# Performance work log

Hardware: AMD Instinct MI355X
Metric: run time of the kernel (lower is better)

The kernel has to match this reference:

```python
import math
import jax, jax.numpy as jnp
import numpy as np

SHAPES = ((100, 150), (50, 75), (25, 38), (13, 19))  # (H, W) per level
N_HEADS = 8
N_POINTS = 4
EMBED = 256


def setup_inputs() -> dict:
    key = jax.random.key(0)
    ks = jax.random.split(key, 8)
    bs = 2
    L = len(SHAPES)
    nv = sum(h * w for h, w in SHAPES)  # 19947
    nq = nv
    d = EMBED
    query = jax.random.normal(ks[0], (bs, nq, d), jnp.float32)
    value = jax.random.normal(ks[1], (bs, nv, d), jnp.float32)
    reference_points = jax.random.uniform(ks[2], (bs, nq, L, 2), dtype=jnp.float32)
    spatial_shapes = jnp.asarray(np.array(SHAPES, np.int32))
    # sampling_offsets bias: directional grid init, as in the module's init_weights
    thetas = np.arange(N_HEADS, dtype=np.float64) * (2.0 * math.pi / N_HEADS)
    grid = np.stack([np.cos(thetas), np.sin(thetas)], -1)
    grid = grid / np.abs(grid).max(-1, keepdims=True)
    grid = np.tile(grid[:, None, None, :], (1, L, N_POINTS, 1))
    grid = grid * np.arange(1, N_POINTS + 1, dtype=np.float64)[None, None, :, None]
    b_off = jnp.asarray(grid.reshape(-1), jnp.float32)  # (h*L*p*2,)
    # small random weights (zero-init in module would make offsets constant)
    W_off = 0.01 * jax.random.normal(ks[3], (N_HEADS * L * N_POINTS * 2, d), jnp.float32)
    W_attn = 0.01 * jax.random.normal(ks[4], (N_HEADS * L * N_POINTS, d), jnp.float32)
    b_attn = jnp.zeros((N_HEADS * L * N_POINTS,), jnp.float32)
    s = 1.0 / math.sqrt(d)
    W_val = s * jax.random.normal(ks[5], (d, d), jnp.float32)
    b_val = jnp.zeros((d,), jnp.float32)
    W_out = s * jax.random.normal(ks[6], (d, d), jnp.float32)
    b_out = jnp.zeros((d,), jnp.float32)
    return dict(query=query, value=value, reference_points=reference_points,
                spatial_shapes=spatial_shapes, W_off=W_off, b_off=b_off,
                W_attn=W_attn, b_attn=b_attn, W_val=W_val, b_val=b_val,
                W_out=W_out, b_out=b_out)


def _msda(value, shapes, loc, attn):
    """Multi-scale deformable attention core.
    value: (bs, nv, h, hd)  loc: (bs, nq, h, L, p, 2) in [0,1]
    attn:  (bs, nq, h, L, p) -> returns (bs, nq, h*hd)
    Equivalent to grid_sample(bilinear, padding='zeros', align_corners=False).
    """
    bs, nq, h, L, p, _ = loc.shape
    hd = value.shape[-1]
    out = jnp.zeros((bs, nq, h, hd), value.dtype)
    start = 0
    for lvl in range(L):
        H, W = int(shapes[lvl, 0]), int(shapes[lvl, 1])
        v = value[:, start:start + H * W]               # (bs, H*W, h, hd)
        l = loc[:, :, :, lvl]                           # (bs, nq, h, p, 2)
        # align_corners=False unnormalization: x = loc*W - 0.5
        x = l[..., 0] * W - 0.5
        y = l[..., 1] * H - 0.5
        x0 = jnp.floor(x)
        y0 = jnp.floor(y)
        wx = x - x0
        wy = y - y0
        x0i = x0.astype(jnp.int32)
        y0i = y0.astype(jnp.int32)

        def corner(xi, yi, w):
            valid = (xi >= 0) & (xi < W) & (yi >= 0) & (yi < H)
            idx = jnp.clip(yi, 0, H - 1) * W + jnp.clip(xi, 0, W - 1)  # (bs,nq,h,p)
            idxf = idx.transpose(0, 1, 3, 2).reshape(bs, nq * p, h)
            g = jnp.take_along_axis(v, idxf[..., None], axis=1)        # (bs,nq*p,h,hd)
            g = g.reshape(bs, nq, p, h, hd).transpose(0, 1, 3, 2, 4)   # (bs,nq,h,p,hd)
            return g * jnp.where(valid, w, 0.0)[..., None]

        samp = (corner(x0i, y0i, (1 - wx) * (1 - wy))
                + corner(x0i + 1, y0i, wx * (1 - wy))
                + corner(x0i, y0i + 1, (1 - wx) * wy)
                + corner(x0i + 1, y0i + 1, wx * wy))
        out = out + (samp * attn[:, :, :, lvl, :, None]).sum(3)
        start += H * W
    return out.reshape(bs, nq, h * hd)


def reference(query, value, reference_points, spatial_shapes,
              W_off, b_off, W_attn, b_attn, W_val, b_val, W_out, b_out):
    shapes = np.asarray(spatial_shapes)  # static level shapes
    bs, nq, d = query.shape
    L = shapes.shape[0]
    h, p = N_HEADS, N_POINTS
    hd = d // h
    off = (query @ W_off.T + b_off).reshape(bs, nq, h, L, p, 2)
    aw = (query @ W_attn.T + b_attn).reshape(bs, nq, h, L * p)
    aw = jax.nn.softmax(aw, axis=-1).reshape(bs, nq, h, L, p)
    v = (value @ W_val.T + b_val).reshape(bs, -1, h, hd)
    # offset normalizer is (W, H) per level
    norm = jnp.asarray(np.stack([shapes[:, 1], shapes[:, 0]], -1), query.dtype)  # (L,2)
    loc = reference_points[:, :, None, :, None, :] + off / norm[None, None, None, :, None, :]
    out = _msda(v, shapes, loc, aw)          # (bs, nq, d)
    return out @ W_out.T + b_out
```

## Files before the change

kernel.cpp:

```cpp
#include <hip/hip_runtime.h>
#include <hip/hip_bf16.h>
#include <hip/hip_fp16.h>
#include <cmath>


typedef __attribute__((ext_vector_type(8))) short short8;
typedef __attribute__((ext_vector_type(4))) float f32x4;

#define MREAL 39894
#define MP    39936
#define NQ2   39894

__device__ __forceinline__ unsigned short f2bf(float f) {
    union { float f; unsigned u; } x; x.f = f;
    unsigned r = (x.u + 0x7fffu + ((x.u >> 16) & 1u)) >> 16;
    return (unsigned short)r;
}
__device__ __forceinline__ unsigned cvt_pk_bf16(float lo, float hi) {
    unsigned r;
    asm("v_cvt_pk_bf16_f32 %0, %1, %2" : "=v"(r) : "v"(lo), "v"(hi));
    return r;
}

template<int AMODE, int OUTMODE>
__device__ __forceinline__ void gemm_body(
    short* As, short* Bs,
    const void* A, const float* B1, const float* B2, int nsplit,
    const float* bias, const float* bias2, int bsplit,
    void* Cout, int ldc, int m_t, int n_t, int Mstore)
{
    const int tid = threadIdx.x;
    const int m0 = m_t * 128;
    const int n0 = n_t * 128;
    const int w  = tid >> 6;
    const int l  = tid & 63;
    const int wm = w >> 1, wn = w & 1;

    const int sr  = tid >> 2;
    const int skc = (tid & 3) * 8;

    const int lr = l & 15;
    const int lk = (l >> 4) * 8;

    const int br0 = n0 + sr, br1 = n0 + sr + 64;
    const float* Bp0 = (br0 < nsplit) ? B1 + (size_t)br0 * 256
                                      : B2 + (size_t)(br0 - nsplit) * 256;
    const float* Bp1 = (br1 < nsplit) ? B1 + (size_t)br1 * 256
                                      : B2 + (size_t)(br1 - nsplit) * 256;

    f32x4 acc[4][4] = {};

    for (int k0 = 0; k0 < 256; k0 += 32) {
        __syncthreads();
        if constexpr (AMODE == 0) {
            const short* Ab = (const short*)A;
            *reinterpret_cast<short8*>(&As[sr * 40 + skc]) =
                *reinterpret_cast<const short8*>(&Ab[(size_t)(m0 + sr) * 256 + k0 + skc]);
            *reinterpret_cast<short8*>(&As[(sr + 64) * 40 + skc]) =
                *reinterpret_cast<const short8*>(&Ab[(size_t)(m0 + sr + 64) * 256 + k0 + skc]);
        } else {
            const float* Af = (const float*)A;
            const int r0 = min(m0 + sr, MREAL - 1);
            const int r1 = min(m0 + sr + 64, MREAL - 1);
            float4 a0 = *reinterpret_cast<const float4*>(&Af[(size_t)r0 * 256 + k0 + skc]);
            float4 a1 = *reinterpret_cast<const float4*>(&Af[(size_t)r0 * 256 + k0 + skc + 4]);
            float4 b0 = *reinterpret_cast<const float4*>(&Af[(size_t)r1 * 256 + k0 + skc]);
            float4 b1 = *reinterpret_cast<const float4*>(&Af[(size_t)r1 * 256 + k0 + skc + 4]);
            uint4 pa, pb;
            pa.x = cvt_pk_bf16(a0.x, a0.y); pa.y = cvt_pk_bf16(a0.z, a0.w);
            pa.z = cvt_pk_bf16(a1.x, a1.y); pa.w = cvt_pk_bf16(a1.z, a1.w);
            pb.x = cvt_pk_bf16(b0.x, b0.y); pb.y = cvt_pk_bf16(b0.z, b0.w);
            pb.z = cvt_pk_bf16(b1.x, b1.y); pb.w = cvt_pk_bf16(b1.z, b1.w);
            *reinterpret_cast<uint4*>(&As[sr * 40 + skc]) = pa;
            *reinterpret_cast<uint4*>(&As[(sr + 64) * 40 + skc]) = pb;
        }
        {
            float4 c0 = *reinterpret_cast<const float4*>(Bp0 + k0 + skc);
            float4 c1 = *reinterpret_cast<const float4*>(Bp0 + k0 + skc + 4);
            float4 d0 = *reinterpret_cast<const float4*>(Bp1 + k0 + skc);
            float4 d1 = *reinterpret_cast<const float4*>(Bp1 + k0 + skc + 4);
            uint4 pc, pd;
            pc.x = cvt_pk_bf16(c0.x, c0.y); pc.y = cvt_pk_bf16(c0.z, c0.w);
            pc.z = cvt_pk_bf16(c1.x, c1.y); pc.w = cvt_pk_bf16(c1.z, c1.w);
            pd.x = cvt_pk_bf16(d0.x, d0.y); pd.y = cvt_pk_bf16(d0.z, d0.w);
            pd.z = cvt_pk_bf16(d1.x, d1.y); pd.w = cvt_pk_bf16(d1.z, d1.w);
            *reinterpret_cast<uint4*>(&Bs[sr * 40 + skc]) = pc;
            *reinterpret_cast<uint4*>(&Bs[(sr + 64) * 40 + skc]) = pd;
        }
        __syncthreads();

        short8 bfr[4];
#pragma unroll
        for (int ni = 0; ni < 4; ++ni)
            bfr[ni] = *reinterpret_cast<const short8*>(&Bs[(wn * 64 + ni * 16 + lr) * 40 + lk]);
#pragma unroll
        for (int mi = 0; mi < 4; ++mi) {
            short8 afr = *reinterpret_cast<const short8*>(&As[(wm * 64 + mi * 16 + lr) * 40 + lk]);
#pragma unroll
            for (int ni = 0; ni < 4; ++ni)
                acc[mi][ni] = __builtin_amdgcn_mfma_f32_16x16x32_bf16(afr, bfr[ni], acc[mi][ni], 0, 0, 0);
        }
    }

    const int r4 = (l >> 4) * 4;
#pragma unroll
    for (int ni = 0; ni < 4; ++ni) {
        const int col = n0 + wn * 64 + ni * 16 + lr;
        const float bv = (col < bsplit) ? bias[col] : bias2[col - bsplit];
#pragma unroll
        for (int mi = 0; mi < 4; ++mi) {
#pragma unroll
            for (int r = 0; r < 4; ++r) {
                const int row = m0 + wm * 64 + mi * 16 + r4 + r;
                if (row < Mstore) {
                    const float val = acc[mi][ni][r] + bv;
                    if constexpr (OUTMODE == 2) {
                        union { __half h; unsigned short u; } cv; cv.h = __float2half(val);
                        reinterpret_cast<unsigned short*>(Cout)[(size_t)row * ldc + col] = cv.u;
                    } else if constexpr (OUTMODE == 3) {
                        union { __half h; unsigned short u; } cv; cv.h = __float2half(val);
                        reinterpret_cast<unsigned short*>(Cout)[(size_t)(col >> 5) * MP * 32
                                                               + (size_t)row * 32 + (col & 31)] = cv.u;
                    } else {
                        reinterpret_cast<float*>(Cout)[(size_t)row * ldc + col] = val;
                    }
                }
            }
        }
    }
}

__global__ __launch_bounds__(256) void gemm_fused(
    const float* __restrict__ value, const float* __restrict__ query,
    const float* __restrict__ woff, const float* __restrict__ wattn,
    const float* __restrict__ wval,
    const float* __restrict__ b_off, const float* __restrict__ b_attn,
    const float* __restrict__ b_val,
    short* __restrict__ vplanes, short* __restrict__ oabuf)
{
    __shared__ short As[128 * 40];
    __shared__ short Bs[128 * 40];

    const int bid = blockIdx.x;
    if (bid < 624) {
        const int m_t = ((bid >> 4) << 3) | (bid & 7);
        const int n_t = (bid >> 3) & 1;
        gemm_body<1, 3>(As, Bs, value, wval, wval, 256,
                        b_val, b_val, 1 << 30, vplanes, 256, m_t, n_t, MP);
    } else {
        const int b = bid - 624;
        const int m_t = ((b / 24) << 3) | (b & 7);
        const int n_t = (b >> 3) % 3;
        gemm_body<1, 2>(As, Bs, query, woff, wattn, 256,
                        b_off, b_attn, 256, oabuf, 384, m_t, n_t, MP);
    }
}

__global__ __launch_bounds__(256) void gemm_out(
    const short* __restrict__ sbuf, const float* __restrict__ wout,
    const float* __restrict__ b_out, float* __restrict__ out)
{
    __shared__ short As[128 * 40];
    __shared__ short Bs[128 * 40];
    const int bid = blockIdx.x;
    const int m_t = ((bid >> 4) << 3) | (bid & 7);
    const int n_t = (bid >> 3) & 1;
    gemm_body<0, 0>(As, Bs, sbuf, wout, wout, 256,
                    b_out, b_out, 1 << 30, out, 256, m_t, n_t, MREAL);
}

__global__ __launch_bounds__(256) void msda_sample7(
    const char* __restrict__ vplanes,
    const __half* __restrict__ offattn,
    const float* __restrict__ ref,
    uint4* __restrict__ sampled)
{
    __shared__ __attribute__((aligned(16))) unsigned s_w[16][68];
    __shared__ __attribute__((aligned(16))) int      s_idx[16][68];
    __shared__ float s_inv[16];

    const int bid = blockIdx.x;
    const int h = bid & 7;
    const int qbase = (bid >> 3) * 16;
    const int tid = threadIdx.x;
    const int qp = tid >> 4;

    {
        const int s = tid & 15;
        const int lvl = s >> 2;
        const int qi = qbase + qp;
        const bool live = (qi < NQ2);

        const int Hs[4] = {100, 50, 25, 13};
        const int Ws[4] = {150, 75, 38, 19};
        const int st[4] = {0, 15000, 18750, 19700};

        float e = 1.f;
        unsigned wv[4] = {0, 0, 0, 0};
        int      iv[4] = {0, 0, 0, 0};
        if (live) {
            const __half* oa = offattn + (size_t)qi * 384;
            unsigned short lu = __builtin_nontemporal_load(
                reinterpret_cast<const unsigned short*>(oa + 256 + h * 16 + s));
            union { unsigned short u; __half h; } lh; lh.u = lu;
            e = __expf(__half2float(lh.h));
            unsigned ou = __builtin_nontemporal_load(
                reinterpret_cast<const unsigned*>(oa + h * 32 + 2 * s));
            union { unsigned u; __half2 h2; } oh; oh.u = ou;
            const float ox = __low2float(oh.h2), oy = __high2float(oh.h2);
            const float2 r2 = *reinterpret_cast<const float2*>(ref + (size_t)qi * 8 + lvl * 2);

            const int H = Hs[lvl], W = Ws[lvl];
            const float x = r2.x * (float)W + ox - 0.5f;
            const float y = r2.y * (float)H + oy - 0.5f;
            const float x0f = floorf(x), y0f = floorf(y);
            const float wx = x - x0f, wy = y - y0f;
            const int x0 = (int)x0f, y0 = (int)y0f;
            const int base = ((qi >= 19947) ? 19947 : 0) + st[lvl];

            const float w00 = (1.f - wx) * (1.f - wy), w01 = wx * (1.f - wy);
            const float w10 = (1.f - wx) * wy,         w11 = wx * wy;
            const bool vx0 = (x0 >= 0) & (x0 < W), vx1 = (x0 + 1 >= 0) & (x0 + 1 < W);
            const bool vy0 = (y0 >= 0) & (y0 < H), vy1 = (y0 + 1 >= 0) & (y0 + 1 < H);
            const int xc0 = min(max(x0, 0), W - 1), xc1 = min(max(x0 + 1, 0), W - 1);
            const int yc0 = min(max(y0, 0), H - 1), yc1 = min(max(y0 + 1, 0), H - 1);
            iv[0] = (base + yc0 * W + xc0) << 6;
            iv[1] = (base + yc0 * W + xc1) << 6;
            iv[2] = (base + yc1 * W + xc0) << 6;
            iv[3] = (base + yc1 * W + xc1) << 6;
            union { __half2 h; unsigned u; } cw;
            cw.h = __float2half2_rn((vx0 & vy0) ? e * w00 : 0.f); wv[0] = cw.u;
            cw.h = __float2half2_rn((vx1 & vy0) ? e * w01 : 0.f); wv[1] = cw.u;
            cw.h = __float2half2_rn((vx0 & vy1) ? e * w10 : 0.f); wv[2] = cw.u;
            cw.h = __float2half2_rn((vx1 & vy1) ? e * w11 : 0.f); wv[3] = cw.u;
        }
        float den = e;
        den += __shfl_xor(den, 1, 64);
        den += __shfl_xor(den, 2, 64);
        den += __shfl_xor(den, 4, 64);
        den += __shfl_xor(den, 8, 64);
        if (s == 0) s_inv[qp] = 1.f / den;
#pragma unroll
        for (int c = 0; c < 4; ++c) {
            s_w[qp][c * 16 + s] = wv[c];
            s_idx[qp][c * 16 + s] = iv[c];
        }
    }
    __syncthreads();

    const int l = tid & 63;
    const int c4 = (l >> 2) & 3;
    const int cp4 = l & 3;
    const int qi = qbase + qp;

    const char* vb = vplanes + (size_t)h * (MP * 64) + cp4 * 16;

    const unsigned* wp = &s_w[qp][c4 * 16];
    const int*      ip = &s_idx[qp][c4 * 16];

    const int4 ia = *reinterpret_cast<const int4*>(ip + 0);
    const int4 ib = *reinterpret_cast<const int4*>(ip + 4);
    const int4 ic = *reinterpret_cast<const int4*>(ip + 8);
    const int4 id = *reinterpret_cast<const int4*>(ip + 12);
    const uint4 wa = *reinterpret_cast<const uint4*>(wp + 0);
    const uint4 wb = *reinterpret_cast<const uint4*>(wp + 4);
    const uint4 wc = *reinterpret_cast<const uint4*>(wp + 8);
    const uint4 wd = *reinterpret_cast<const uint4*>(wp + 12);

    const uint4 p0  = *reinterpret_cast<const uint4*>(vb + ia.x);
    const uint4 p1  = *reinterpret_cast<const uint4*>(vb + ia.y);
    const uint4 p2  = *reinterpret_cast<const uint4*>(vb + ia.z);
    const uint4 p3  = *reinterpret_cast<const uint4*>(vb + ia.w);
    const uint4 p4  = *reinterpret_cast<const uint4*>(vb + ib.x);
    const uint4 p5  = *reinterpret_cast<const uint4*>(vb + ib.y);
    const uint4 p6  = *reinterpret_cast<const uint4*>(vb + ib.z);
    const uint4 p7  = *reinterpret_cast<const uint4*>(vb + ib.w);
    const uint4 p8  = *reinterpret_cast<const uint4*>(vb + ic.x);
    const uint4 p9  = *reinterpret_cast<const uint4*>(vb + ic.y);
    const uint4 p10 = *reinterpret_cast<const uint4*>(vb + ic.z);
    const uint4 p11 = *reinterpret_cast<const uint4*>(vb + ic.w);
    const uint4 p12 = *reinterpret_cast<const uint4*>(vb + id.x);
    const uint4 p13 = *reinterpret_cast<const uint4*>(vb + id.y);
    const uint4 p14 = *reinterpret_cast<const uint4*>(vb + id.z);
    const uint4 p15 = *reinterpret_cast<const uint4*>(vb + id.w);

    union HU { __half2 h; unsigned u; };
    __half2 acc[4];
#pragma unroll
    for (int i = 0; i < 4; ++i) acc[i] = __float2half2_rn(0.f);

#define FMA4(P, WU) { HU va, ww; ww.u = (WU); \
    va.u = (P).x; acc[0] = __hfma2(va.h, ww.h, acc[0]); \
    va.u = (P).y; acc[1] = __hfma2(va.h, ww.h, acc[1]); \
    va.u = (P).z; acc[2] = __hfma2(va.h, ww.h, acc[2]); \
    va.u = (P).w; acc[3] = __hfma2(va.h, ww.h, acc[3]); }

    FMA4(p0,  wa.x) FMA4(p1,  wa.y) FMA4(p2,  wa.z) FMA4(p3,  wa.w)
    FMA4(p4,  wb.x) FMA4(p5,  wb.y) FMA4(p6,  wb.z) FMA4(p7,  wb.w)
    FMA4(p8,  wc.x) FMA4(p9,  wc.y) FMA4(p10, wc.z) FMA4(p11, wc.w)
    FMA4(p12, wd.x) FMA4(p13, wd.y) FMA4(p14, wd.z) FMA4(p15, wd.w)
#undef FMA4

#pragma unroll
    for (int i = 0; i < 4; ++i) {
        HU a; a.h = acc[i];
        HU b;
        b.u = __shfl_xor(a.u, 4, 64); a.h = __hadd2(a.h, b.h);
        b.u = __shfl_xor(a.u, 8, 64); a.h = __hadd2(a.h, b.h);
        acc[i] = a.h;
    }

    if (c4 == 0 && qi < NQ2) {
        const float inv = s_inv[qp];
        uint4 o;
        o.x = ((unsigned)f2bf(__high2float(acc[0]) * inv) << 16) | (unsigned)f2bf(__low2float(acc[0]) * inv);
        o.y = ((unsigned)f2bf(__high2float(acc[1]) * inv) << 16) | (unsigned)f2bf(__low2float(acc[1]) * inv);
        o.z = ((unsigned)f2bf(__high2float(acc[2]) * inv) << 16) | (unsigned)f2bf(__low2float(acc[2]) * inv);
        o.w = ((unsigned)f2bf(__high2float(acc[3]) * inv) << 16) | (unsigned)f2bf(__low2float(acc[3]) * inv);
        sampled[(size_t)qi * 32 + h * 4 + cp4] = o;
    }
}

extern "C" void kernel_launch(void* const* d_in, const int* in_sizes, int n_in,
                              void* d_out, int out_size, void* d_ws, size_t ws_size,
                              hipStream_t stream) {
    const float* query  = (const float*)d_in[0];
    const float* value  = (const float*)d_in[1];
    const float* refp   = (const float*)d_in[2];
    const float* W_off  = (const float*)d_in[4];
    const float* b_off  = (const float*)d_in[5];
    const float* W_attn = (const float*)d_in[6];
    const float* b_attn = (const float*)d_in[7];
    const float* W_val  = (const float*)d_in[8];
    const float* b_val  = (const float*)d_in[9];
    const float* W_out  = (const float*)d_in[10];
    const float* b_out  = (const float*)d_in[11];
    float* out = (float*)d_out;

    short* vplanes = (short*)d_ws;
    short* oabuf   = vplanes + (size_t)MP * 256;
    short* sbuf    = oabuf + (size_t)MP * 384;

    const dim3 blk(256);

    gemm_fused<<<dim3(624 + 936), blk, 0, stream>>>(
        value, query, W_off, W_attn, W_val, b_off, b_attn, b_val, vplanes, oabuf);

    const int ngroups = (MREAL + 15) / 16;
    msda_sample7<<<dim3(ngroups * 8), blk, 0, stream>>>(
        (const char*)vplanes, (const __half*)oabuf, refp, (uint4*)sbuf);

    gemm_out<<<dim3(624), blk, 0, stream>>>(sbuf, W_out, b_out, out);
}
```

Measured before the change: 140.0 us.

## Restructure GEMM tiles: 512 threads, register-prefetched A, half-K staged B

The GEMM body now runs with 512 threads, 8 waves in a 2x4 arrangement, so each wave computes a 64x32 sub-tile instead of 64x64. A tiles are prefetched into registers one k-step ahead and written to LDS after compute. B is loaded once per half-K (128 wide) into a larger LDS buffer rather than every k-step. The aim is to overlap global loads with MFMA work and cut repeated B conversion traffic, at the cost of more LDS per block, two barriers per k-step, and a change in occupancy.

```diff
diff --git a/kernel.cpp b/kernel.cpp
--- a/kernel.cpp
+++ b/kernel.cpp
@@ -24,88 +24,99 @@
 
 template<int AMODE, int OUTMODE>
 __device__ __forceinline__ void gemm_body(
-    short* As, short* Bs,
-    const void* A, const float* B1, const float* B2, int nsplit,
-    const float* bias, const float* bias2, int bsplit,
-    void* Cout, int ldc, int m_t, int n_t, int Mstore)
+    short* __restrict__ As, short* __restrict__ Bs,
+    const void* __restrict__ A, const float* __restrict__ B1,
+    const float* __restrict__ B2, int nsplit,
+    const float* __restrict__ bias, const float* __restrict__ bias2, int bsplit,
+    void* __restrict__ Cout, int ldc, int m_t, int n_t, int Mstore)
 {
     const int tid = threadIdx.x;
     const int m0 = m_t * 128;
     const int n0 = n_t * 128;
     const int w  = tid >> 6;
     const int l  = tid & 63;
-    const int wm = w >> 1, wn = w & 1;
-
-    const int sr  = tid >> 2;
-    const int skc = (tid & 3) * 8;
-
+    const int wm = w >> 2, wn = w & 3;
     const int lr = l & 15;
     const int lk = (l >> 4) * 8;
 
-    const int br0 = n0 + sr, br1 = n0 + sr + 64;
-    const float* Bp0 = (br0 < nsplit) ? B1 + (size_t)br0 * 256
-                                      : B2 + (size_t)(br0 - nsplit) * 256;
-    const float* Bp1 = (br1 < nsplit) ? B1 + (size_t)br1 * 256
-                                      : B2 + (size_t)(br1 - nsplit) * 256;
-
-    f32x4 acc[4][4] = {};
-
-    for (int k0 = 0; k0 < 256; k0 += 32) {
-        __syncthreads();
-        if constexpr (AMODE == 0) {
+    const int srow = tid >> 2;
+    const int skc  = (tid & 3) * 8;
+    const int bkc  = (tid & 3) * 32;
+
+    const int gn = n0 + srow;
+    const float* Bp = (gn < nsplit) ? B1 + (size_t)gn * 256
+                                    : B2 + (size_t)(gn - nsplit) * 256;
+
+    f32x4 acc[4][2] = {};
+
+    float4 pa0, pa1;
+    short8 pab;
+
+    auto loadA = [&](int ks) {
+        if constexpr (AMODE == 1) {
+            const float* Af = (const float*)A;
+            const int r = min(m0 + srow, MREAL - 1);
+            const float* p = Af + (size_t)r * 256 + ks * 32 + skc;
+            pa0 = *reinterpret_cast<const float4*>(p);
+            pa1 = *reinterpret_cast<const float4*>(p + 4);
+        } else {
             const short* Ab = (const short*)A;
-            *reinterpret_cast<short8*>(&As[sr * 40 + skc]) =
-                *reinterpret_cast<const short8*>(&Ab[(size_t)(m0 + sr) * 256 + k0 + skc]);
-            *reinterpret_cast<short8*>(&As[(sr + 64) * 40 + skc]) =
-                *reinterpret_cast<const short8*>(&Ab[(size_t)(m0 + sr + 64) * 256 + k0 + skc]);
+            pab = *reinterpret_cast<const short8*>(Ab + (size_t)(m0 + srow) * 256 + ks * 32 + skc);
+        }
+    };
+    auto writeA = [&]() {
+        if constexpr (AMODE == 1) {
+            uint4 q;
+            q.x = cvt_pk_bf16(pa0.x, pa0.y); q.y = cvt_pk_bf16(pa0.z, pa0.w);
+            q.z = cvt_pk_bf16(pa1.x, pa1.y); q.w = cvt_pk_bf16(pa1.z, pa1.w);
+            *reinterpret_cast<uint4*>(&As[srow * 40 + skc]) = q;
         } else {
-            const float* Af = (const float*)A;
-            const int r0 = min(m0 + sr, MREAL - 1);
-            const int r1 = min(m0 + sr + 64, MREAL - 1);
-            float4 a0 = *reinterpret_cast<const float4*>(&Af[(size_t)r0 * 256 + k0 + skc]);
-            float4 a1 = *reinterpret_cast<const float4*>(&Af[(size_t)r0 * 256 + k0 + skc + 4]);
-            float4 b0 = *reinterpret_cast<const float4*>(&Af[(size_t)r1 * 256 + k0 + skc]);
-            float4 b1 = *reinterpret_cast<const float4*>(&Af[(size_t)r1 * 256 + k0 + skc + 4]);
-            uint4 pa, pb;
-            pa.x = cvt_pk_bf16(a0.x, a0.y); pa.y = cvt_pk_bf16(a0.z, a0.w);
-            pa.z = cvt_pk_bf16(a1.x, a1.y); pa.w = cvt_pk_bf16(a1.z, a1.w);
-            pb.x = cvt_pk_bf16(b0.x, b0.y); pb.y = cvt_pk_bf16(b0.z, b0.w);
-            pb.z = cvt_pk_bf16(b1.x, b1.y); pb.w = cvt_pk_bf16(b1.z, b1.w);
-            *reinterpret_cast<uint4*>(&As[sr * 40 + skc]) = pa;
-            *reinterpret_cast<uint4*>(&As[(sr + 64) * 40 + skc]) = pb;
-        }
-        {
-            float4 c0 = *reinterpret_cast<const float4*>(Bp0 + k0 + skc);
-            float4 c1 = *reinterpret_cast<const float4*>(Bp0 + k0 + skc + 4);
-            float4 d0 = *reinterpret_cast<const float4*>(Bp1 + k0 + skc);
-            float4 d1 = *reinterpret_cast<const float4*>(Bp1 + k0 + skc + 4);
-            uint4 pc, pd;
-            pc.x = cvt_pk_bf16(c0.x, c0.y); pc.y = cvt_pk_bf16(c0.z, c0.w);
-            pc.z = cvt_pk_bf16(c1.x, c1.y); pc.w = cvt_pk_bf16(c1.z, c1.w);
-            pd.x = cvt_pk_bf16(d0.x, d0.y); pd.y = cvt_pk_bf16(d0.z, d0.w);
-            pd.z = cvt_pk_bf16(d1.x, d1.y); pd.w = cvt_pk_bf16(d1.z, d1.w);
-            *reinterpret_cast<uint4*>(&Bs[sr * 40 + skc]) = pc;
-            *reinterpret_cast<uint4*>(&Bs[(sr + 64) * 40 + skc]) = pd;
-        }
-        __syncthreads();
-
-        short8 bfr[4];
-#pragma unroll
-        for (int ni = 0; ni < 4; ++ni)
-            bfr[ni] = *reinterpret_cast<const short8*>(&Bs[(wn * 64 + ni * 16 + lr) * 40 + lk]);
+            *reinterpret_cast<short8*>(&As[srow * 40 + skc]) = pab;
+        }
+    };
+    auto loadB = [&](int half) {
+        const float* p = Bp + half * 128 + bkc;
+#pragma unroll
+        for (int i = 0; i < 4; ++i) {
+            float4 x = *reinterpret_cast<const float4*>(p + i * 8);
+            float4 y = *reinterpret_cast<const float4*>(p + i * 8 + 4);
+            uint4 q;
+            q.x = cvt_pk_bf16(x.x, x.y); q.y = cvt_pk_bf16(x.z, x.w);
+            q.z = cvt_pk_bf16(y.x, y.y); q.w = cvt_pk_bf16(y.z, y.w);
+            *reinterpret_cast<uint4*>(&Bs[srow * 136 + bkc + i * 8]) = q;
+        }
+    };
+
+    loadB(0);
+    loadA(0);
+    writeA();
+    loadA(1);
+    __syncthreads();
+
+#pragma unroll
+    for (int ks = 0; ks < 8; ++ks) {
+        const int kk = (ks & 3) * 32;
+        short8 bfr0 = *reinterpret_cast<const short8*>(&Bs[(wn * 32 + lr) * 136 + kk + lk]);
+        short8 bfr1 = *reinterpret_cast<const short8*>(&Bs[(wn * 32 + 16 + lr) * 136 + kk + lk]);
 #pragma unroll
         for (int mi = 0; mi < 4; ++mi) {
             short8 afr = *reinterpret_cast<const short8*>(&As[(wm * 64 + mi * 16 + lr) * 40 + lk]);
-#pragma unroll
-            for (int ni = 0; ni < 4; ++ni)
-                acc[mi][ni] = __builtin_amdgcn_mfma_f32_16x16x32_bf16(afr, bfr[ni], acc[mi][ni], 0, 0, 0);
+            acc[mi][0] = __builtin_amdgcn_mfma_f32_16x16x32_bf16(afr, bfr0, acc[mi][0], 0, 0, 0);
+            acc[mi][1] = __builtin_amdgcn_mfma_f32_16x16x32_bf16(afr, bfr1, acc[mi][1], 0, 0, 0);
+        }
+        if (ks < 7) {
+            __syncthreads();
+            writeA();
+            if (ks == 3) loadB(1);
+            if (ks < 6) loadA(ks + 2);
+            __syncthreads();
         }
     }
 
     const int r4 = (l >> 4) * 4;
 #pragma unroll
-    for (int ni = 0; ni < 4; ++ni) {
-        const int col = n0 + wn * 64 + ni * 16 + lr;
+    for (int ni = 0; ni < 2; ++ni) {
+        const int col = n0 + wn * 32 + ni * 16 + lr;
         const float bv = (col < bsplit) ? bias[col] : bias2[col - bsplit];
 #pragma unroll
         for (int mi = 0; mi < 4; ++mi) {
@@ -130,7 +141,7 @@
     }
 }
 
-__global__ __launch_bounds__(256) void gemm_fused(
+__global__ __launch_bounds__(512) void gemm_fused(
     const float* __restrict__ value, const float* __restrict__ query,
     const float* __restrict__ woff, const float* __restrict__ wattn,
     const float* __restrict__ wval,
@@ -139,7 +150,7 @@
     short* __restrict__ vplanes, short* __restrict__ oabuf)
 {
     __shared__ short As[128 * 40];
-    __shared__ short Bs[128 * 40];
+    __shared__ short Bs[128 * 136];
 
     const int bid = blockIdx.x;
     if (bid < 624) {
@@ -156,12 +167,12 @@
     }
 }
 
-__global__ __launch_bounds__(256) void gemm_out(
+__global__ __launch_bounds__(512) void gemm_out(
     const short* __restrict__ sbuf, const float* __restrict__ wout,
     const float* __restrict__ b_out, float* __restrict__ out)
 {
     __shared__ short As[128 * 40];
-    __shared__ short Bs[128 * 40];
+    __shared__ short Bs[128 * 136];
     const int bid = blockIdx.x;
     const int m_t = ((bid >> 4) << 3) | (bid & 7);
     const int n_t = (bid >> 3) & 1;
@@ -341,14 +352,12 @@
     short* oabuf   = vplanes + (size_t)MP * 256;
     short* sbuf    = oabuf + (size_t)MP * 384;
 
-    const dim3 blk(256);
-
-    gemm_fused<<<dim3(624 + 936), blk, 0, stream>>>(
+    gemm_fused<<<dim3(624 + 936), dim3(512), 0, stream>>>(
         value, query, W_off, W_attn, W_val, b_off, b_attn, b_val, vplanes, oabuf);
 
     const int ngroups = (MREAL + 15) / 16;
-    msda_sample7<<<dim3(ngroups * 8), blk, 0, stream>>>(
+    msda_sample7<<<dim3(ngroups * 8), dim3(256), 0, stream>>>(
         (const char*)vplanes, (const __half*)oabuf, refp, (uint4*)sbuf);
 
-    gemm_out<<<dim3(624), blk, 0, stream>>>(sbuf, W_out, b_out, out);
-}
+    gemm_out<<<dim3(624), dim3(512), 0, stream>>>(sbuf, W_out, b_out, out);
+}
```

Measured after the change: 147.0 us. 1.05x slower.
